# Optimization experiments

Hardware: AMD Instinct MI355X
Metric: run time of the kernel (lower is better)

## Reference

```python
import jax, jax.numpy as jnp
import numpy as np

E4M3_MAX = 448.0
IGNORE = -1000.0
ROTARY_BASE = 10000.0


def quant_dequant_e4m3(w):
    """Emulate per-tensor FP8 E4M3 quantize->dequantize (3 mantissa bits, max 448)."""
    amax = jnp.max(jnp.abs(w))
    scale = E4M3_MAX / jnp.maximum(amax, 1e-12)
    v = w * scale
    a = jnp.abs(v)
    # exponent clipped to E4M3 range (min normal exp -6, max 8)
    e = jnp.clip(jnp.floor(jnp.log2(jnp.maximum(a, 1e-30))), -6.0, 8.0)
    step = jnp.exp2(e - 3.0)  # 3 mantissa bits
    q = jnp.clip(jnp.round(v / step) * step, -E4M3_MAX, E4M3_MAX)
    return (q / scale).astype(w.dtype)


def rotary_sin_cos(rotary_dim, n_ctx):
    pos = jnp.arange(n_ctx, dtype=jnp.float32)
    dim = jnp.arange(rotary_dim // 2, dtype=jnp.float32)
    inv_freq = ROTARY_BASE ** (-dim / (rotary_dim / 2))
    ang = pos[:, None] * inv_freq[None, :]            # [n_ctx, rotary_dim//2]
    ang = jnp.concatenate([ang, ang], axis=-1)        # [n_ctx, rotary_dim]
    return jnp.sin(ang), jnp.cos(ang)


def apply_rotary(x, sin, cos, rotary_dim):
    # x: [B, S, H, Dh]; rotate first rotary_dim dims with rotate-half convention
    S = x.shape[1]
    x_rot, x_pass = x[..., :rotary_dim], x[..., rotary_dim:]
    half = rotary_dim // 2
    x_flip = jnp.concatenate([-x_rot[..., half:], x_rot[..., :half]], axis=-1)
    c = cos[:S][None, :, None, :]
    s = sin[:S][None, :, None, :]
    out = x_rot * c + x_flip * s
    return jnp.concatenate([out, x_pass], axis=-1) if rotary_dim < x.shape[-1] else out


def setup_inputs() -> dict:
    key = jax.random.key(0)
    ks = jax.random.split(key, 8)
    B, S, D, H, Dh = 2, 2048, 1024, 16, 64
    return {
        "query_input": jax.random.normal(ks[0], (B, S, D), jnp.float32),
        "key_input": jax.random.normal(ks[1], (B, S, D), jnp.float32),
        "value_input": jax.random.normal(ks[2], (B, S, D), jnp.float32),
        "W_Q": jax.random.normal(ks[3], (H, D, Dh), jnp.float32) * 0.02,
        "W_K": jax.random.normal(ks[4], (H, D, Dh), jnp.float32) * 0.02,
        "W_V": jax.random.normal(ks[5], (H, D, Dh), jnp.float32) * 0.02,
        "W_O": jax.random.normal(ks[6], (H, Dh, D), jnp.float32) * 0.02,
        "b_Q": jnp.zeros((H, Dh), jnp.float32),
        "b_K": jnp.zeros((H, Dh), jnp.float32),
        "b_V": jnp.zeros((H, Dh), jnp.float32),
        "b_O": jnp.zeros((D,), jnp.float32),
    }


def reference(query_input, key_input, value_input, W_Q, W_K, W_V, W_O, b_Q, b_K, b_V, b_O):
    B, S, D = query_input.shape
    H, _, Dh = W_Q.shape
    rotary_dim = Dh
    attn_scale = jnp.sqrt(jnp.asarray(Dh, jnp.float32))

    # FP8-quantized QKV weights/biases (E4M3 quant-dequant emulation)
    Wq = quant_dequant_e4m3(W_Q)
    Wk = quant_dequant_e4m3(W_K)
    Wv = quant_dequant_e4m3(W_V)
    bq = quant_dequant_e4m3(b_Q)
    bk = quant_dequant_e4m3(b_K)
    bv = quant_dequant_e4m3(b_V)

    q = jnp.einsum("bsd,hde->bshe", query_input, Wq) + bq  # [B,S,H,Dh]
    k = jnp.einsum("bsd,hde->bshe", key_input, Wk) + bk
    v = jnp.einsum("bsd,hde->bshe", value_input, Wv) + bv

    sin, cos = rotary_sin_cos(rotary_dim, S)
    q = apply_rotary(q, sin, cos, rotary_dim)
    k = apply_rotary(k, sin, cos, rotary_dim)

    scores = jnp.einsum("bqhe,bkhe->bhqk", q, k) / attn_scale  # [B,H,S,S]
    causal = jnp.tril(jnp.ones((S, S), bool))
    scores = jnp.where(causal[None, None], scores, IGNORE)
    pattern = jax.nn.softmax(scores, axis=-1)

    z = jnp.einsum("bhqk,bkhe->bqhe", pattern, v)             # [B,S,H,Dh]
    out = jnp.einsum("bqhe,hed->bqd", z, W_O) + b_O           # [B,S,D]
    return out
```

## Files before the change

### kernel.cpp

```cpp
#include <hip/hip_runtime.h>
#include <math.h>


typedef __attribute__((ext_vector_type(8))) short bf16x8;
typedef __attribute__((ext_vector_type(16))) float f32x16;
typedef __attribute__((ext_vector_type(4))) float f32x4;
typedef __attribute__((ext_vector_type(4))) float f4;

#define E4M3_MAX 448.0f

__device__ inline float bf2f(ushort u) { return __uint_as_float(((unsigned)u) << 16); }
__device__ inline ushort f2bf(float f) {
  unsigned u = __float_as_uint(f);
  return (ushort)((u + 0x7FFF + ((u >> 16) & 1)) >> 16);
}
__device__ inline unsigned pack2bf(float a, float b) {
  unsigned ua = __float_as_uint(a), ub = __float_as_uint(b);
  return ((ua + 0x8000u) >> 16) | ((ub + 0x8000u) & 0xFFFF0000u);
}

__device__ __forceinline__ void gll16(const ushort* g, ushort* l) {
  __builtin_amdgcn_global_load_lds(
      (const __attribute__((address_space(1))) unsigned int*)g,
      (__attribute__((address_space(3))) unsigned int*)l, 16, 0, 0);
}

__device__ inline float qdq_qval(float w, float amax) {
  float scale = E4M3_MAX / fmaxf(amax, 1e-12f);
  float v = w * scale;
  float a = fmaxf(fabsf(v), 1e-30f);
  int ex;
  (void)frexpf(a, &ex);
  float e = fminf(fmaxf((float)(ex - 1), -6.0f), 8.0f);
  float step = exp2f(e - 3.0f);
  float q = rintf(v / step) * step;
  return fminf(fmaxf(q, -E4M3_MAX), E4M3_MAX);
}

__device__ __forceinline__ float redpart64(const float* __restrict__ p, int tid) {
  float v = p[tid & 63];
  #pragma unroll
  for (int o = 32; o > 0; o >>= 1) v = fmaxf(v, __shfl_xor(v, o));
  return v;
}

__global__ __launch_bounds__(256) void prep1(const float* __restrict__ W0,
                                             const float* __restrict__ W1,
                                             const float* __restrict__ W2,
                                             const float* __restrict__ b0,
                                             const float* __restrict__ b1,
                                             const float* __restrict__ b2,
                                             const float* __restrict__ Xq,
                                             const float* __restrict__ Xk,
                                             const float* __restrict__ Xv,
                                             float* __restrict__ amaxpart,
                                             ushort* __restrict__ xq,
                                             ushort* __restrict__ xk,
                                             ushort* __restrict__ xv) {
  __shared__ float wred[4];
  int bid = blockIdx.x, tid = threadIdx.x;
  if (bid < 384) {
    int y = bid >> 6, xb = bid & 63;
    const float* src = (y == 0) ? W0 : (y == 1) ? W1 : (y == 2) ? W2
                     : (y == 3) ? b0 : (y == 4) ? b1 : b2;
    int n = (y < 3) ? 1048576 : 1024;
    float m = 0.0f;
    for (int i = xb * 256 + tid; i < n; i += 64 * 256)
      m = fmaxf(m, fabsf(src[i]));
    #pragma unroll
    for (int off = 32; off > 0; off >>= 1)
      m = fmaxf(m, __shfl_xor(m, off));
    if ((tid & 63) == 0) wred[tid >> 6] = m;
    __syncthreads();
    if (tid == 0)
      amaxpart[y * 64 + xb] = fmaxf(fmaxf(wred[0], wred[1]), fmaxf(wred[2], wred[3]));
  } else {
    int t = bid - 384;
    int y = t >> 12, xb = t & 4095;
    const float* in = (y == 0) ? Xq : (y == 1) ? Xk : Xv;
    ushort* out = (y == 0) ? xq : (y == 1) ? xk : xv;
    int i = xb * 256 + tid;
    f4 v = *(const f4*)(in + (size_t)i * 4);
    uint2 o;
    o.x = (unsigned)f2bf(v[0]) | ((unsigned)f2bf(v[1]) << 16);
    o.y = (unsigned)f2bf(v[2]) | ((unsigned)f2bf(v[3]) << 16);
    *(uint2*)(out + (size_t)i * 4) = o;
  }
}

__global__ __launch_bounds__(256) void prep2(const float* __restrict__ W0,
                                             const float* __restrict__ W1,
                                             const float* __restrict__ W2,
                                             const float* __restrict__ WO,
                                             const float* __restrict__ b0,
                                             const float* __restrict__ b1,
                                             const float* __restrict__ b2,
                                             const float* __restrict__ amaxpart,
                                             float* __restrict__ amax,
                                             ushort* __restrict__ o0,
                                             ushort* __restrict__ o1,
                                             ushort* __restrict__ o2,
                                             ushort* __restrict__ woT,
                                             float* __restrict__ bq,
                                             float* __restrict__ bk,
                                             float* __restrict__ bv) {
  __shared__ float tile[64][65];
  int bid = blockIdx.x, tid = threadIdx.x;
  if (bid < 768) {
    int z = bid >> 8, r = bid & 255, hh = r >> 4, xb = r & 15;
    const float* W = (z == 0) ? W0 : (z == 1) ? W1 : W2;
    ushort* Bt = (z == 0) ? o0 : (z == 1) ? o1 : o2;
    float am = redpart64(amaxpart + z * 64, tid);
    if (r == 0 && tid == 0) amax[z] = am;
    int d0 = xb * 64;
    int e = tid & 63, dd = tid >> 6;
    #pragma unroll
    for (int p = 0; p < 16; p++)
      tile[dd + p * 4][e] = W[(size_t)hh * 65536 + (size_t)(d0 + dd + p * 4) * 64 + e];
    __syncthreads();
    int d = tid & 63, ee = tid >> 6;
    #pragma unroll
    for (int p = 0; p < 16; p++) {
      int e2 = ee + p * 4;
      Bt[(size_t)(hh * 64 + e2) * 1024 + d0 + d] = f2bf(qdq_qval(tile[d][e2], am));
    }
  } else if (bid < 780) {
    int q = bid - 768, y = q >> 2, xb = q & 3;
    const float* b = (y == 0) ? b0 : (y == 1) ? b1 : b2;
    float* o = (y == 0) ? bq : (y == 1) ? bk : bv;
    float am = redpart64(amaxpart + (3 + y) * 64, tid);
    int idx = xb * 256 + tid;
    if (idx < 1024) {
      float qv = qdq_qval(b[idx], am);
      o[idx] = qv * (fmaxf(am, 1e-12f) * (1.0f / E4M3_MAX));
    }
  } else {
    int t = bid - 780;
    int xb = t & 15, yb = t >> 4;
    int d0 = xb * 64, he0 = yb * 64;
    int dcol = tid & 63, hr = tid >> 6;
    #pragma unroll
    for (int p = 0; p < 16; p++)
      tile[hr + p * 4][dcol] = WO[(size_t)(he0 + hr + p * 4) * 1024 + d0 + dcol];
    __syncthreads();
    int hcol = tid & 63, dr = tid >> 6;
    #pragma unroll
    for (int p = 0; p < 16; p++)
      woT[(size_t)(d0 + dr + p * 4) * 1024 + he0 + hcol] = f2bf(tile[hcol][dr + p * 4]);
  }
}

template <int MODE, int TN>
__device__ __forceinline__ void gemm_body(const ushort* __restrict__ A,
                                          const ushort* __restrict__ Bt,
                                          const float* __restrict__ bias, float s_inv,
                                          ushort* __restrict__ outb, float* __restrict__ outf,
                                          int bx, int by, ushort* As, ushort* Bs) {
  const int K = 1024, N = 1024;
  const int JF = TN / 32;
  int tid = threadIdx.x;
  int w = tid >> 6, lane = tid & 63, quad = lane >> 4, l16 = lane & 15;
  int wm = w & 1, wn = w >> 1;
  int row0 = by * 128, col0 = bx * TN;
  f32x4 acc[4][4] = {};

  for (int k0 = 0; k0 < K; k0 += 64) {
    __syncthreads();
    {
      #pragma unroll
      for (int p = 0; p < 4; p++) {
        int u = tid + p * 256;
        int r = u >> 3, c = u & 7, cs = c ^ (r & 7);
        gll16(&A[(size_t)(row0 + r) * K + k0 + cs * 8], &As[u * 8]);
      }
      #pragma unroll
      for (int p = 0; p < TN / 32; p++) {
        int u = tid + p * 256;
        int r = u >> 3, c = u & 7, cs = c ^ (r & 7);
        gll16(&Bt[(size_t)(col0 + r) * K + k0 + cs * 8], &Bs[u * 8]);
      }
    }
    __syncthreads();
    #pragma unroll
    for (int kk = 0; kk < 2; kk++) {
      bf16x8 af[4], bfr[JF];
      #pragma unroll
      for (int i = 0; i < 4; i++) {
        int arow = wm * 64 + i * 16 + l16;
        af[i] = *(const bf16x8*)&As[arow * 64 + (((kk * 4 + quad) ^ (arow & 7)) * 8)];
      }
      #pragma unroll
      for (int j = 0; j < JF; j++) {
        int brow = wn * (TN / 2) + j * 16 + l16;
        bfr[j] = *(const bf16x8*)&Bs[brow * 64 + (((kk * 4 + quad) ^ (brow & 7)) * 8)];
      }
      #pragma unroll
      for (int i = 0; i < 4; i++)
        #pragma unroll
        for (int j = 0; j < JF; j++)
          acc[i][j] = __builtin_amdgcn_mfma_f32_16x16x32_bf16(af[i], bfr[j], acc[i][j], 0, 0, 0);
    }
  }

  if (MODE == 2) {
    float bv0[4];
    #pragma unroll
    for (int j = 0; j < 4; j++) bv0[j] = bias[col0 + wn * 64 + j * 16 + l16];
    #pragma unroll
    for (int jp = 0; jp < 2; jp++) {
      float invf = exp2f((float)(jp * 16 + l16) * (-13.287712379549449f / 32.0f));
      int collo = col0 + wn * 64 + jp * 16 + l16;
      #pragma unroll
      for (int i = 0; i < 4; i++) {
        #pragma unroll
        for (int r = 0; r < 4; r++) {
          int row = row0 + wm * 64 + i * 16 + quad * 4 + r;
          float ang = (float)(row & 2047) * invf;
          float sn = __sinf(ang), c = __cosf(ang);
          float lo = acc[i][jp][r] * s_inv + bv0[jp];
          float hi = acc[i][jp + 2][r] * s_inv + bv0[jp + 2];
          outb[(size_t)row * N + collo] = f2bf(lo * c - hi * sn);
          outb[(size_t)row * N + collo + 32] = f2bf(hi * c + lo * sn);
        }
      }
    }
  } else if (MODE == 3) {
    __syncthreads();
    ushort* sb = As;
    #pragma unroll
    for (int j = 0; j < JF; j++) {
      int colL = wn * (TN / 2) + j * 16 + l16;
      float bv = bias[col0 + colL];
      #pragma unroll
      for (int i = 0; i < 4; i++) {
        int rowL = wm * 64 + i * 16 + quad * 4;
        uint2 o;
        o.x = (unsigned)f2bf(acc[i][j][0] * s_inv + bv) |
              ((unsigned)f2bf(acc[i][j][1] * s_inv + bv) << 16);
        o.y = (unsigned)f2bf(acc[i][j][2] * s_inv + bv) |
              ((unsigned)f2bf(acc[i][j][3] * s_inv + bv) << 16);
        *(uint2*)&sb[colL * 136 + rowL] = o;
      }
    }
    __syncthreads();
    int bb = row0 >> 11, sloc = row0 & 2047;
    #pragma unroll
    for (int p = 0; p < 8; p++) {
      int u = tid + p * 256;
      int r = u >> 4, cc = u & 15;
      *(uint4*)&outb[(size_t)(bb * 1024 + col0 + r) * 2048 + sloc + cc * 8] =
          *(const uint4*)&sb[r * 136 + cc * 8];
    }
  } else {
    #pragma unroll
    for (int j = 0; j < JF; j++) {
      int col = col0 + wn * (TN / 2) + j * 16 + l16;
      float bv = bias[col];
      #pragma unroll
      for (int i = 0; i < 4; i++) {
        int row = row0 + wm * 64 + i * 16 + quad * 4;
        #pragma unroll
        for (int r = 0; r < 4; r++)
          outf[(size_t)(row + r) * N + col] = acc[i][j][r] * s_inv + bv;
      }
    }
  }
}

__global__ __launch_bounds__(256) void gemm3_qkv(const ushort* __restrict__ xq,
                                                 const ushort* __restrict__ xk,
                                                 const ushort* __restrict__ xv,
                                                 const ushort* __restrict__ wq,
                                                 const ushort* __restrict__ wk,
                                                 const ushort* __restrict__ wv,
                                                 const float* __restrict__ bq,
                                                 const float* __restrict__ bk,
                                                 const float* __restrict__ bv,
                                                 const float* __restrict__ amax,
                                                 ushort* __restrict__ oq,
                                                 ushort* __restrict__ ok,
                                                 ushort* __restrict__ vT) {
  __shared__ __align__(16) ushort sb[17408];
  ushort* As = sb;
  ushort* Bs = sb + 8192;
  int bid = blockIdx.x;
  int rr = bid & 7, t = bid >> 3;
  int bx = t & 7, gq = rr + 8 * (t >> 3);
  int by = gq & 31, z = gq >> 5;
  const ushort* A  = (z == 0) ? xq : (z == 1) ? xk : xv;
  const ushort* Bt = (z == 0) ? wq : (z == 1) ? wk : wv;
  const float* bias = (z == 0) ? bq : (z == 1) ? bk : bv;
  float s_inv = fmaxf(amax[z], 1e-12f) * (1.0f / E4M3_MAX);
  if (z == 2)
    gemm_body<3, 128>(A, Bt, bias, s_inv, vT, nullptr, bx, by, As, Bs);
  else
    gemm_body<2, 128>(A, Bt, bias, s_inv, (z == 0) ? oq : ok, nullptr, bx, by, As, Bs);
}

__global__ __launch_bounds__(256) void gemm_wo(const ushort* __restrict__ A,
                                               const ushort* __restrict__ Bt,
                                               const float* __restrict__ bias,
                                               float* __restrict__ out) {
  __shared__ __align__(16) ushort As[8192], Bs[4096];
  int bid = blockIdx.x;
  int rr = bid & 7, t = bid >> 3;
  int bx = t & 15, by = rr + 8 * (t >> 4);
  gemm_body<0, 64>(A, Bt, bias, 1.0f, nullptr, out, bx, by, As, Bs);
}

__global__ __launch_bounds__(512, 4) void flash_mfma9(const ushort* __restrict__ qb,
                                                      const ushort* __restrict__ kb,
                                                      const ushort* __restrict__ vT,
                                                      ushort* __restrict__ zb) {
  int h = blockIdx.y, b = blockIdx.z;
  int tid = threadIdx.x;
  int w8 = tid >> 6;
  int g = w8 >> 2;
  int w = w8 & 3;
  int lane = tid & 63, h2 = lane >> 5, l31 = lane & 31;
  __shared__ ushort sbuf[16384 + 18432];
  ushort* Ks = sbuf + g * 4096;
  ushort* Vs = sbuf + 8192 + g * 4096;
  ushort* P2 = sbuf + 16384 + g * 9216;

  const int qrow = w * 32 + l31;
  const float CE = 0.125f;

  const int ts = tid & 255;
  const int u0 = ts, u1 = ts + 256;
  const int r0 = u0 >> 3, c0 = u0 & 7, r1 = u1 >> 3, c1 = u1 & 7;
  const int sw0 = (c0 ^ (r0 & 7)) * 8, sw1 = (c1 ^ (r1 & 7)) * 8;

  const int qt = (blockIdx.z == 0) ? (int)blockIdx.x : 15 - (int)blockIdx.x;
  const int q0 = qt * 128;
  const int qg = q0 + w * 32 + l31;
  size_t qbase = ((size_t)(b * 2048 + qg)) * 1024 + (size_t)h * 64;
  bf16x8 qf[4];
  #pragma unroll
  for (int ck = 0; ck < 4; ck++)
    qf[ck] = *(const bf16x8*)&qb[qbase + ck * 16 + h2 * 8];

  f32x16 accO[2] = {};
  float mrun = -INFINITY, lrun = 0.0f;

  const int nt = qt + 1;
  const int kt0 = g * nt;

  const ushort* ksrc0 = kb + ((size_t)(b * 2048 + kt0 * 64 + r0)) * 1024 + (size_t)h * 64 + c0 * 8;
  const ushort* ksrc1 = kb + ((size_t)(b * 2048 + kt0 * 64 + r1)) * 1024 + (size_t)h * 64 + c1 * 8;
  const ushort* vsrc0 = vT + ((size_t)((b * 16 + h) * 64 + r0)) * 2048 + kt0 * 64 + c0 * 8;
  const ushort* vsrc1 = vT + ((size_t)((b * 16 + h) * 64 + r1)) * 2048 + kt0 * 64 + c1 * 8;

  uint4 kc0 = *(const uint4*)ksrc0;
  uint4 kc1 = *(const uint4*)ksrc1;
  uint4 vc0 = *(const uint4*)vsrc0;
  uint4 vc1 = *(const uint4*)vsrc1;

  for (int t = 0; t < nt; t++) {
    int kt = kt0 + t;
    __syncthreads();
    *(uint4*)&Ks[r0 * 64 + sw0] = kc0;
    *(uint4*)&Ks[r1 * 64 + sw1] = kc1;
    *(uint4*)&Vs[r0 * 64 + sw0] = vc0;
    *(uint4*)&Vs[r1 * 64 + sw1] = vc1;
    __syncthreads();
    if (t + 1 < nt) {
      kc0 = *(const uint4*)(ksrc0 + (size_t)(t + 1) * 65536);
      kc1 = *(const uint4*)(ksrc1 + (size_t)(t + 1) * 65536);
      vc0 = *(const uint4*)(vsrc0 + (t + 1) * 64);
      vc1 = *(const uint4*)(vsrc1 + (t + 1) * 64);
    }

    bool active = (kt * 64 <= q0 + w * 32 + 31);
    if (active) {
      f32x16 sc[2] = {};
      #pragma unroll
      for (int mf = 0; mf < 2; mf++) {
        int row = mf * 32 + l31;
        int s8 = row & 7;
        #pragma unroll
        for (int ck = 0; ck < 4; ck++) {
          bf16x8 ka = *(const bf16x8*)&Ks[row * 64 + (((2 * ck + h2) ^ s8) * 8)];
          sc[mf] = __builtin_amdgcn_mfma_f32_32x32x16_bf16(ka, qf[ck], sc[mf], 0, 0, 0);
        }
      }

      if (kt * 64 + 63 > q0 + w * 32) {
        #pragma unroll
        for (int mf = 0; mf < 2; mf++)
          #pragma unroll
          for (int i = 0; i < 16; i++) {
            int kv = kt * 64 + mf * 32 + (i & 3) + 8 * (i >> 2) + 4 * h2;
            sc[mf][i] = (kv > qg) ? -8000.0f : sc[mf][i];
          }
      }

      float tm = sc[0][0];
      #pragma unroll
      for (int i = 1; i < 16; i++) tm = fmaxf(tm, sc[0][i]);
      #pragma unroll
      for (int i = 0; i < 16; i++) tm = fmaxf(tm, sc[1][i]);
      tm = fmaxf(tm, __shfl_xor(tm, 32));
      float mnew = fmaxf(mrun, tm);
      float alpha = __expf((mrun - mnew) * CE);
      float p[2][16];
      float rs = 0.0f;
      #pragma unroll
      for (int mf = 0; mf < 2; mf++)
        #pragma unroll
        for (int i = 0; i < 16; i++) {
          float pv = __expf((sc[mf][i] - mnew) * CE);
          p[mf][i] = pv;
          rs += pv;
        }
      rs += __shfl_xor(rs, 32);
      lrun = lrun * alpha + rs;
      mrun = mnew;
      #pragma unroll
      for (int mf = 0; mf < 2; mf++)
        #pragma unroll
        for (int i = 0; i < 16; i++) accO[mf][i] *= alpha;

      #pragma unroll
      for (int mf = 0; mf < 2; mf++)
        #pragma unroll
        for (int m = 0; m < 4; m++) {
          uint2 w2;
          w2.x = pack2bf(p[mf][4 * m + 0], p[mf][4 * m + 1]);
          w2.y = pack2bf(p[mf][4 * m + 2], p[mf][4 * m + 3]);
          *(uint2*)&P2[qrow * 72 + 32 * mf + 8 * m + 4 * h2] = w2;
        }

      #pragma unroll
      for (int ck = 0; ck < 4; ck++) {
        bf16x8 pB = *(const bf16x8*)&P2[qrow * 72 + ck * 16 + h2 * 8];
        #pragma unroll
        for (int mf = 0; mf < 2; mf++) {
          int row = mf * 32 + l31;
          bf16x8 va = *(const bf16x8*)&Vs[row * 64 + (((2 * ck + h2) ^ (row & 7)) * 8)];
          accO[mf] = __builtin_amdgcn_mfma_f32_32x32x16_bf16(va, pB, accO[mf], 0, 0, 0);
        }
      }
    }
  }

  __syncthreads();
  float* mbuf = (float*)sbuf;
  int midx = (w * 64 + lane) * 35;
  if (g == 1) {
    #pragma unroll
    for (int i = 0; i < 16; i++) mbuf[midx + i] = accO[0][i];
    #pragma unroll
    for (int i = 0; i < 16; i++) mbuf[midx + 16 + i] = accO[1][i];
    mbuf[midx + 32] = mrun;
    mbuf[midx + 33] = lrun;
  }
  __syncthreads();
  ushort* Osb = sbuf + 16384 + 9216;
  if (g == 0) {
    float m1 = mbuf[midx + 32], l1 = mbuf[midx + 33];
    float mn = fmaxf(mrun, m1);
    float a0 = __expf((mrun - mn) * CE), a1 = __expf((m1 - mn) * CE);
    float linv = 1.0f / (lrun * a0 + l1 * a1);
    #pragma unroll
    for (int mf = 0; mf < 2; mf++)
      #pragma unroll
      for (int m = 0; m < 4; m++) {
        int e0 = 32 * mf + 8 * m + 4 * h2;
        float o0 = (accO[mf][4 * m + 0] * a0 + mbuf[midx + 16 * mf + 4 * m + 0] * a1) * linv;
        float o1 = (accO[mf][4 * m + 1] * a0 + mbuf[midx + 16 * mf + 4 * m + 1] * a1) * linv;
        float o2 = (accO[mf][4 * m + 2] * a0 + mbuf[midx + 16 * mf + 4 * m + 2] * a1) * linv;
        float o3 = (accO[mf][4 * m + 3] * a0 + mbuf[midx + 16 * mf + 4 * m + 3] * a1) * linv;
        *(unsigned*)&Osb[qrow * 72 + e0] = pack2bf(o0, o1);
        *(unsigned*)&Osb[qrow * 72 + e0 + 2] = pack2bf(o2, o3);
      }
  }
  __syncthreads();
  size_t obase = ((size_t)(b * 2048 + q0)) * 1024 + (size_t)h * 64;
  #pragma unroll
  for (int i = 0; i < 2; i++) {
    int u = tid + i * 512;
    int r = u >> 3, blk = u & 7;
    *(uint4*)&zb[obase + (size_t)r * 1024 + blk * 8] = *(const uint4*)&Osb[r * 72 + blk * 8];
  }
}

extern "C" void kernel_launch(void* const* d_in, const int* in_sizes, int n_in,
                              void* d_out, int out_size, void* d_ws, size_t ws_size,
                              hipStream_t stream) {
  const float* Xq  = (const float*)d_in[0];
  const float* Xk  = (const float*)d_in[1];
  const float* Xv  = (const float*)d_in[2];
  const float* W_Q = (const float*)d_in[3];
  const float* W_K = (const float*)d_in[4];
  const float* W_V = (const float*)d_in[5];
  const float* W_O = (const float*)d_in[6];
  const float* b_Q = (const float*)d_in[7];
  const float* b_K = (const float*)d_in[8];
  const float* b_V = (const float*)d_in[9];
  const float* b_O = (const float*)d_in[10];
  float* out = (float*)d_out;

  char* base = (char*)d_ws;
  float*  amax = (float*)(base + 0);
  float*  amaxpart = (float*)(base + 1024);
  float*  bq   = (float*)(base + 4096);
  float*  bk   = (float*)(base + 8192);
  float*  bv   = (float*)(base + 12288);
  ushort* wq   = (ushort*)(base + 16384);
  ushort* wk   = (ushort*)(base + 16384 + 2097152);
  ushort* wv   = (ushort*)(base + 16384 + 2u * 2097152);
  ushort* woT  = (ushort*)(base + 16384 + 3u * 2097152);
  ushort* xq   = (ushort*)(base + 8404992);
  ushort* xk   = (ushort*)(base + 16793600);
  ushort* xv   = (ushort*)(base + 25182208);
  ushort* qbf  = (ushort*)(base + 33570816);
  ushort* kbf  = (ushort*)(base + 41959424);
  ushort* vT   = (ushort*)(base + 50348032);
  ushort* zbf  = xk;

  prep1<<<12672, 256, 0, stream>>>(W_Q, W_K, W_V, b_Q, b_K, b_V, Xq, Xk, Xv,
                                   amaxpart, xq, xk, xv);
  prep2<<<1036, 256, 0, stream>>>(W_Q, W_K, W_V, W_O, b_Q, b_K, b_V,
                                  amaxpart, amax, wq, wk, wv, woT, bq, bk, bv);
  gemm3_qkv<<<768, 256, 0, stream>>>(xq, xk, xv, wq, wk, wv, bq, bk, bv, amax,
                                     qbf, kbf, vT);
  dim3 fgrid(16, 16, 2);
  flash_mfma9<<<fgrid, 512, 0, stream>>>(qbf, kbf, vT, zbf);
  gemm_wo<<<512, 256, 0, stream>>>(zbf, woT, b_O, out);
}
```

Before: 229.0 us.

## Keep softmax probabilities in registers via permlane32 swap instead of LDS round-trip

The flash attention kernel no longer writes the bf16 probability tile to shared memory and reads it back as the MFMA B operand. Instead it packs probabilities into registers and rearranges them across the two half-waves with permlane32_swap, falling back to shuffles if the builtin is missing. It also switches the exponentials to native exp2 with a folded log2e scale and uses tree reductions for the row max and row sum to shorten dependency chains. This removes LDS traffic and a store-load hazard per tile, at the cost of relying on the swap semantics matching the MFMA operand layout.

```diff
diff --git a/kernel.cpp b/kernel.cpp
--- a/kernel.cpp
+++ b/kernel.cpp
@@ -9,6 +9,12 @@
 
 #define E4M3_MAX 448.0f
 
+#if __has_builtin(__builtin_amdgcn_exp2f)
+#define FEXP2(x) __builtin_amdgcn_exp2f(x)
+#else
+#define FEXP2(x) exp2f(x)
+#endif
+
 __device__ inline float bf2f(ushort u) { return __uint_as_float(((unsigned)u) << 16); }
 __device__ inline ushort f2bf(float f) {
   unsigned u = __float_as_uint(f);
@@ -17,6 +23,22 @@
 __device__ inline unsigned pack2bf(float a, float b) {
   unsigned ua = __float_as_uint(a), ub = __float_as_uint(b);
   return ((ua + 0x8000u) >> 16) | ((ub + 0x8000u) & 0xFFFF0000u);
+}
+
+__device__ __forceinline__ void pl32swap(unsigned& a, unsigned& b, int h2) {
+#if __has_builtin(__builtin_amdgcn_permlane32_swap)
+  typedef __attribute__((ext_vector_type(2))) int i32x2;
+  i32x2 r = __builtin_amdgcn_permlane32_swap((int)a, (int)b, false, false);
+  a = (unsigned)r[0];
+  b = (unsigned)r[1];
+#else
+  unsigned pa = (unsigned)__shfl_xor((int)a, 32);
+  unsigned pb = (unsigned)__shfl_xor((int)b, 32);
+  unsigned na = h2 ? pb : a;
+  unsigned nb = h2 ? b : pa;
+  a = na;
+  b = nb;
+#endif
 }
 
 __device__ __forceinline__ void gll16(const ushort* g, ushort* l) {
@@ -308,10 +330,10 @@
   gemm_body<0, 64>(A, Bt, bias, 1.0f, nullptr, out, bx, by, As, Bs);
 }
 
-__global__ __launch_bounds__(512, 4) void flash_mfma9(const ushort* __restrict__ qb,
-                                                      const ushort* __restrict__ kb,
-                                                      const ushort* __restrict__ vT,
-                                                      ushort* __restrict__ zb) {
+__global__ __launch_bounds__(512, 4) void flash_mfma10(const ushort* __restrict__ qb,
+                                                       const ushort* __restrict__ kb,
+                                                       const ushort* __restrict__ vT,
+                                                       ushort* __restrict__ zb) {
   int h = blockIdx.y, b = blockIdx.z;
   int tid = threadIdx.x;
   int w8 = tid >> 6;
@@ -321,10 +343,10 @@
   __shared__ ushort sbuf[16384 + 18432];
   ushort* Ks = sbuf + g * 4096;
   ushort* Vs = sbuf + 8192 + g * 4096;
-  ushort* P2 = sbuf + 16384 + g * 9216;
 
   const int qrow = w * 32 + l31;
   const float CE = 0.125f;
+  const float SCL = 0.180336880f;
 
   const int ts = tid & 255;
   const int u0 = ts, u1 = ts + 256;
@@ -395,25 +417,38 @@
           }
       }
 
-      float tm = sc[0][0];
-      #pragma unroll
-      for (int i = 1; i < 16; i++) tm = fmaxf(tm, sc[0][i]);
-      #pragma unroll
-      for (int i = 0; i < 16; i++) tm = fmaxf(tm, sc[1][i]);
-      tm = fmaxf(tm, __shfl_xor(tm, 32));
+      float mx[16];
+      #pragma unroll
+      for (int i = 0; i < 16; i++) mx[i] = fmaxf(sc[0][i], sc[1][i]);
+      #pragma unroll
+      for (int s2 = 8; s2; s2 >>= 1)
+        #pragma unroll
+        for (int i = 0; i < s2; i++) mx[i] = fmaxf(mx[i], mx[i + s2]);
+      float tm = fmaxf(mx[0], __shfl_xor(mx[0], 32));
       float mnew = fmaxf(mrun, tm);
-      float alpha = __expf((mrun - mnew) * CE);
-      float p[2][16];
-      float rs = 0.0f;
+      float alpha = FEXP2((mrun - mnew) * SCL);
+      float msc = mnew * SCL;
+
+      unsigned pu[2][4], pv[2][4];
+      float sm[16];
       #pragma unroll
       for (int mf = 0; mf < 2; mf++)
         #pragma unroll
-        for (int i = 0; i < 16; i++) {
-          float pv = __expf((sc[mf][i] - mnew) * CE);
-          p[mf][i] = pv;
-          rs += pv;
+        for (int m = 0; m < 4; m++) {
+          float p0 = FEXP2(fmaf(sc[mf][4 * m + 0], SCL, -msc));
+          float p1 = FEXP2(fmaf(sc[mf][4 * m + 1], SCL, -msc));
+          float p2 = FEXP2(fmaf(sc[mf][4 * m + 2], SCL, -msc));
+          float p3 = FEXP2(fmaf(sc[mf][4 * m + 3], SCL, -msc));
+          pu[mf][m] = pack2bf(p0, p1);
+          pv[mf][m] = pack2bf(p2, p3);
+          sm[mf * 8 + m] = p0 + p1;
+          sm[mf * 8 + 4 + m] = p2 + p3;
         }
-      rs += __shfl_xor(rs, 32);
+      #pragma unroll
+      for (int s2 = 8; s2; s2 >>= 1)
+        #pragma unroll
+        for (int i = 0; i < s2; i++) sm[i] += sm[i + s2];
+      float rs = sm[0] + __shfl_xor(sm[0], 32);
       lrun = lrun * alpha + rs;
       mrun = mnew;
       #pragma unroll
@@ -422,23 +457,19 @@
         for (int i = 0; i < 16; i++) accO[mf][i] *= alpha;
 
       #pragma unroll
-      for (int mf = 0; mf < 2; mf++)
-        #pragma unroll
-        for (int m = 0; m < 4; m++) {
-          uint2 w2;
-          w2.x = pack2bf(p[mf][4 * m + 0], p[mf][4 * m + 1]);
-          w2.y = pack2bf(p[mf][4 * m + 2], p[mf][4 * m + 3]);
-          *(uint2*)&P2[qrow * 72 + 32 * mf + 8 * m + 4 * h2] = w2;
-        }
-
-      #pragma unroll
       for (int ck = 0; ck < 4; ck++) {
-        bf16x8 pB = *(const bf16x8*)&P2[qrow * 72 + ck * 16 + h2 * 8];
+        int ms = ck >> 1, cl = ck & 1;
+        unsigned w0 = pu[ms][2 * cl], w2 = pu[ms][2 * cl + 1];
+        unsigned w1 = pv[ms][2 * cl], w3 = pv[ms][2 * cl + 1];
+        pl32swap(w0, w2, h2);
+        pl32swap(w1, w3, h2);
+        union { unsigned u[4]; bf16x8 v8; } pb_;
+        pb_.u[0] = w0; pb_.u[1] = w1; pb_.u[2] = w2; pb_.u[3] = w3;
         #pragma unroll
         for (int mf = 0; mf < 2; mf++) {
           int row = mf * 32 + l31;
           bf16x8 va = *(const bf16x8*)&Vs[row * 64 + (((2 * ck + h2) ^ (row & 7)) * 8)];
-          accO[mf] = __builtin_amdgcn_mfma_f32_32x32x16_bf16(va, pB, accO[mf], 0, 0, 0);
+          accO[mf] = __builtin_amdgcn_mfma_f32_32x32x16_bf16(va, pb_.v8, accO[mf], 0, 0, 0);
         }
       }
     }
@@ -526,6 +557,6 @@
   gemm3_qkv<<<768, 256, 0, stream>>>(xq, xk, xv, wq, wk, wv, bq, bk, bv, amax,
                                      qbf, kbf, vT);
   dim3 fgrid(16, 16, 2);
-  flash_mfma9<<<fgrid, 512, 0, stream>>>(qbf, kbf, vT, zbf);
+  flash_mfma10<<<fgrid, 512, 0, stream>>>(qbf, kbf, vT, zbf);
   gemm_wo<<<512, 256, 0, stream>>>(zbf, woT, b_O, out);
 }
```

Result: no change. 233.0 us (+1.8%).
